# Kernel optimization log

Measured on AMD Instinct MI355X. Metric: run time of the kernel, lower is better.

The kernel has to match this reference:

```python
import jax, jax.numpy as jnp
import numpy as np

D_MODEL = 1024
N_HEAD = 16
DIM_PER_HEAD = D_MODEL // N_HEAD
B, S = 8, 1024


def setup_inputs() -> dict:
    key = jax.random.key(0)
    ks = jax.random.split(key, 12)
    s = 0.02
    return {
        "k": jax.random.normal(ks[0], (B, S, D_MODEL), jnp.float32),
        "v": jax.random.normal(ks[1], (B, S, D_MODEL), jnp.float32),
        "q": jax.random.normal(ks[2], (B, S, D_MODEL), jnp.float32),
        "attn_mask": jax.random.randint(ks[3], (B, S, S), 0, 2, jnp.int32),
        "Wk": jax.random.normal(ks[4], (D_MODEL, D_MODEL), jnp.float32) * s,
        "bk": jnp.zeros((D_MODEL,), jnp.float32),
        "Wv": jax.random.normal(ks[5], (D_MODEL, D_MODEL), jnp.float32) * s,
        "bv": jnp.zeros((D_MODEL,), jnp.float32),
        "Wq": jax.random.normal(ks[6], (D_MODEL, D_MODEL), jnp.float32) * s,
        "bq": jnp.zeros((D_MODEL,), jnp.float32),
        "Wo": jax.random.normal(ks[7], (D_MODEL, D_MODEL), jnp.float32) * s,
        "bo": jnp.zeros((D_MODEL,), jnp.float32),
    }


def reference(k, v, q, attn_mask, Wk, bk, Wv, bv, Wq, bq, Wo, bo):
    batch, key_len, _ = k.shape
    query_len = q.shape[1]
    scale = 1.0 / jnp.sqrt(jnp.float32(DIM_PER_HEAD))

    def split_heads(x):  # [b, s, d] -> [b, h, s, dh]
        return x.reshape(batch, -1, N_HEAD, DIM_PER_HEAD).transpose(0, 2, 1, 3)

    key_up = split_heads(k @ Wk + bk)
    value_up = split_heads(v @ Wv + bv)
    query_up = split_heads(q @ Wq + bq) * scale

    # [b, h, q, k] scores; mask nonzero entries with -inf (masked_fill_ semantics)
    scores = jnp.einsum("bhqd,bhkd->bhqk", query_up, key_up)
    scores = jnp.where(attn_mask[:, None, :, :] != 0, -jnp.inf, scores)
    attn = jax.nn.softmax(scores, axis=-1)
    # NOTE: original applies dropout but discards the result; attn (pre-dropout) is used.
    context = jnp.einsum("bhqk,bhkd->bhqd", attn, value_up)
    context = context.transpose(0, 2, 1, 3).reshape(batch, query_len, D_MODEL)
    output = context @ Wo + bo
    attn_mean = attn.sum(axis=1) / N_HEAD  # [b, q, k]
    return output, attn_mean
```

## Files before the change

kernel.cpp:

```cpp
#include <hip/hip_runtime.h>
#include <hip/hip_bf16.h>

typedef unsigned short u16;
typedef unsigned int u32;
typedef __attribute__((ext_vector_type(8))) short bf16x8;
typedef __attribute__((ext_vector_type(4))) float f32x4;
typedef __attribute__((ext_vector_type(4))) u16 u16x4;
typedef __attribute__((ext_vector_type(4))) u32 u32x4;

#define DEV static __device__ __forceinline__

DEV u16 f2bf(float x) {
  unsigned u = __builtin_bit_cast(unsigned, x);
  u += 0x7fffu + ((u >> 16) & 1u);
  return (u16)(u >> 16);
}
DEV float bf2f(u16 u) { return __builtin_bit_cast(float, ((unsigned)u) << 16); }

DEV u32 cvtpk(float lo, float hi) {
  u32 r;
  asm("v_cvt_pk_bf16_f32 %0, %1, %2" : "=v"(r) : "v"(lo), "v"(hi));
  return r;
}

DEV void glds16(const u16* g, u16* l) {
  __builtin_amdgcn_global_load_lds(
      (const __attribute__((address_space(1))) void*)g,
      (__attribute__((address_space(3))) void*)l, 16, 0, 0);
}

__global__ __launch_bounds__(256) void prep(
    const float* __restrict__ k, const float* __restrict__ v,
    const float* __restrict__ q,
    const float* __restrict__ w0, const float* __restrict__ w1,
    const float* __restrict__ w2, const float* __restrict__ w3,
    const int* __restrict__ mask,
    u16* __restrict__ Xb, u16* __restrict__ WT,
    unsigned long long* __restrict__ Mb) {
  __shared__ u16 tile[32][33];
  const int bid = (int)blockIdx.x;
  const int tid = threadIdx.x;
  if (bid < 2048) {
    const size_t i0 = (size_t)bid * 256 + tid;
    for (size_t t = i0; t < 6291456; t += 524288) {
      const size_t e = t * 4;
      const float* src = (e < 8388608) ? k + e
                       : (e < 16777216) ? v + (e - 8388608)
                       : q + (e - 16777216);
      const f32x4 x = *(const f32x4*)src;
      u16x4 o;
#pragma unroll
      for (int r = 0; r < 4; ++r) o[r] = f2bf(x[r]);
      *(u16x4*)&Xb[e] = o;
    }
  } else if (bid < 6144) {
    const int lb = bid - 2048;
    const int mat = lb >> 10;
    const int bx = lb & 1023;
    const float* in = (mat == 0) ? w0 : (mat == 1) ? w1 : (mat == 2) ? w2 : w3;
    u16* o = WT + (size_t)mat * 1048576;
    const int bk = (bx & 31) << 5;
    const int bn = (bx >> 5) << 5;
    const int tx = tid & 31, ty = tid >> 5;
#pragma unroll
    for (int i = 0; i < 32; i += 8)
      tile[ty + i][tx] = f2bf(in[(size_t)(bk + ty + i) * 1024 + bn + tx]);
    __syncthreads();
#pragma unroll
    for (int i = 0; i < 32; i += 8)
      o[(size_t)(bn + ty + i) * 1024 + bk + tx] = tile[tx][ty + i];
  } else {
    const int lb = bid - 6144;
    const int qt = lb & 63, b = lb >> 6;
    const int w = tid >> 6, l = tid & 63;
    const int ln = l & 15, lg = l >> 4;
    const int* Mp = mask + ((size_t)b << 20) + ((size_t)(qt << 4) << 10);
    unsigned long long m = 0ull;
#pragma unroll
    for (int t = 0; t < 16; ++t) {
      const int key = (w << 8) + (t << 4) + ln;
#pragma unroll
      for (int r = 0; r < 4; ++r) {
        const int row = (lg << 2) + r;
        if (Mp[((size_t)row << 10) + key] != 0) m |= 1ull << ((t << 2) + r);
      }
    }
    Mb[((((size_t)b << 6) + qt) << 8) + tid] = m;
  }
}

__global__ __launch_bounds__(256) void gemm_qkv(
    const u16* __restrict__ Xb, const u16* __restrict__ WTall,
    const float* __restrict__ bK, const float* __restrict__ bV,
    const float* __restrict__ bQ,
    u16* __restrict__ Kup, u16* __restrict__ VupT, u16* __restrict__ Qup) {
  __shared__ u16 As[8192];
  __shared__ u16 Bs[8192];
  const int mode = blockIdx.y;
  const u16* A = Xb + (size_t)mode * 8388608;
  const u16* Bw = WTall + (size_t)mode * 1048576;
  const float* bias = (mode == 0) ? bK : (mode == 1) ? bV : bQ;

  const int tid = threadIdx.x;
  const int w = tid >> 6, l = tid & 63;
  const int ln = l & 15, lg = l >> 4;
  const int wr = w >> 1, wc = w & 1;
  const int mb = ((int)blockIdx.x >> 3) << 7;
  const int nb = ((int)blockIdx.x & 7) << 7;

  f32x4 acc[4][4] = {};
  const int ar = (wr << 6) + ln;
  const int br = (wc << 6) + ln;
  const int x7 = ln & 7;

  for (int k0 = 0; k0 < 1024; k0 += 64) {
#pragma unroll
    for (int i = 0; i < 4; ++i) {
      const int off = (i << 11) + (tid << 3);
      const int row = off >> 6;
      const int sc = ((((off >> 3) & 7) ^ (row & 7)) << 3);
      glds16(A + (size_t)(mb + row) * 1024 + k0 + sc, As + off);
      glds16(Bw + (size_t)(nb + row) * 1024 + k0 + sc, Bs + off);
    }
    __syncthreads();
#pragma unroll
    for (int kk = 0; kk < 2; ++kk) {
      const int g = (kk << 2) + lg;
      const int rc = (g ^ x7) << 3;
      bf16x8 aa[4], bb[4];
#pragma unroll
      for (int mt = 0; mt < 4; ++mt) {
        aa[mt] = *(const bf16x8*)&As[(ar + (mt << 4)) * 64 + rc];
        bb[mt] = *(const bf16x8*)&Bs[(br + (mt << 4)) * 64 + rc];
      }
#pragma unroll
      for (int mt = 0; mt < 4; ++mt)
#pragma unroll
        for (int nt = 0; nt < 4; ++nt)
          acc[mt][nt] = __builtin_amdgcn_mfma_f32_16x16x32_bf16(aa[mt], bb[nt], acc[mt][nt], 0, 0, 0);
    }
    __syncthreads();
  }

  const float scale = (mode == 2) ? 0.125f : 1.0f;
#pragma unroll
  for (int mt = 0; mt < 4; ++mt) {
    const int m0 = mb + (wr << 6) + (mt << 4) + (lg << 2);
    const int bb_ = m0 >> 10, s0 = m0 & 1023;
#pragma unroll
    for (int nt = 0; nt < 4; ++nt) {
      const int n = nb + (wc << 6) + (nt << 4) + ln;
      const float bval = bias[n];
      const int h = n >> 6, dh = n & 63;
      const size_t bh = (size_t)(bb_ * 16 + h);
      if (mode == 1) {
        const int wv = dh >> 4, lnv = dh & 15;
        const int kk = s0 >> 5, lgv = (s0 >> 3) & 3, e0 = s0 & 7;
        u16x4 pk;
#pragma unroll
        for (int r = 0; r < 4; ++r) pk[r] = f2bf(acc[mt][nt][r] + bval);
        *(u16x4*)&VupT[(bh << 16) + (wv << 14) + (kk << 9) + (lgv << 7) +
                       (lnv << 3) + e0] = pk;
      } else if (mode == 0) {
        const int half = dh >> 5, lg2 = (dh >> 3) & 3, e = dh & 7;
        const int T = s0 >> 4;
        u16* base = Kup + (bh << 16) + (T << 10) + (half << 9) + (lg2 << 7) + e;
#pragma unroll
        for (int r = 0; r < 4; ++r)
          base[((s0 & 15) + r) << 3] = f2bf(acc[mt][nt][r] + bval);
      } else {
#pragma unroll
        for (int r = 0; r < 4; ++r)
          Qup[((bh << 10) + s0 + r) * 64 + dh] =
              f2bf((acc[mt][nt][r] + bval) * scale);
      }
    }
  }
}

__global__ __launch_bounds__(256) void gemm_out(
    const u16* __restrict__ Ctx, const u16* __restrict__ WTall,
    const float* __restrict__ bO, const u16* __restrict__ Pp,
    float* __restrict__ Out) {
  __shared__ u16 As[8192];
  __shared__ u16 Bs[8192];
  const int bid = (int)blockIdx.x;
  const int tid = threadIdx.x;

  if (bid >= 512) {
    float* Am = Out + 8388608;
    const size_t i = ((size_t)(bid - 512) * 256 + tid) * 8;
    const u16x4* q0 = (const u16x4*)&Pp[i];
    const u16x4* q1 = (const u16x4*)&Pp[8388608 + i];
    const u16x4 a0 = q0[0], a1 = q0[1], b0 = q1[0], b1 = q1[1];
    f32x4 lo, hi;
#pragma unroll
    for (int r = 0; r < 4; ++r) {
      lo[r] = (bf2f(a0[r]) + bf2f(b0[r])) * 0.0625f;
      hi[r] = (bf2f(a1[r]) + bf2f(b1[r])) * 0.0625f;
    }
    *(f32x4*)&Am[i] = lo;
    *(f32x4*)&Am[i + 4] = hi;
    return;
  }

  const u16* Bw = WTall + 3145728;
  const int w = tid >> 6, l = tid & 63;
  const int ln = l & 15, lg = l >> 4;
  const int wr = w >> 1, wc = w & 1;
  const int mb = (bid >> 3) << 7;
  const int nb = (bid & 7) << 7;

  f32x4 acc[4][4] = {};
  const int ar = (wr << 6) + ln;
  const int br = (wc << 6) + ln;
  const int x7 = ln & 7;

  for (int k0 = 0; k0 < 1024; k0 += 64) {
#pragma unroll
    for (int i = 0; i < 4; ++i) {
      const int off = (i << 11) + (tid << 3);
      const int row = off >> 6;
      const int sc = ((((off >> 3) & 7) ^ (row & 7)) << 3);
      glds16(Ctx + (size_t)(mb + row) * 1024 + k0 + sc, As + off);
      glds16(Bw + (size_t)(nb + row) * 1024 + k0 + sc, Bs + off);
    }
    __syncthreads();
#pragma unroll
    for (int kk = 0; kk < 2; ++kk) {
      const int g = (kk << 2) + lg;
      const int rc = (g ^ x7) << 3;
      bf16x8 aa[4], bb[4];
#pragma unroll
      for (int mt = 0; mt < 4; ++mt) {
        aa[mt] = *(const bf16x8*)&As[(ar + (mt << 4)) * 64 + rc];
        bb[mt] = *(const bf16x8*)&Bs[(br + (mt << 4)) * 64 + rc];
      }
#pragma unroll
      for (int mt = 0; mt < 4; ++mt)
#pragma unroll
        for (int nt = 0; nt < 4; ++nt)
          acc[mt][nt] = __builtin_amdgcn_mfma_f32_16x16x32_bf16(aa[mt], bb[nt], acc[mt][nt], 0, 0, 0);
    }
    __syncthreads();
  }
#pragma unroll
  for (int mt = 0; mt < 4; ++mt) {
    const int m0 = mb + (wr << 6) + (mt << 4) + (lg << 2);
#pragma unroll
    for (int nt = 0; nt < 4; ++nt) {
      const int n = nb + (wc << 6) + (nt << 4) + ln;
      const float bval = bO[n];
#pragma unroll
      for (int r = 0; r < 4; ++r)
        Out[(size_t)(m0 + r) * 1024 + n] = acc[mt][nt][r] + bval;
    }
  }
}

__global__ __launch_bounds__(256, 2) void attn_kernel(
    const u16* __restrict__ Qup, const u16* __restrict__ Kf,
    const u16* __restrict__ Vf, const unsigned long long* __restrict__ Mb,
    u16* __restrict__ Ctx, u16* __restrict__ Pp) {
  __shared__ u16 P_lds[16 * 1024];
  __shared__ float red_s[4][16];
  __shared__ float invs[16];

  const int tid = threadIdx.x;
  const int w = tid >> 6, l = tid & 63;
  const int ln = l & 15, lg = l >> 4;
  const int kg8 = lg << 3;

  const int bid = (int)blockIdx.x;
  const int b = bid & 7;
  const int idx = bid >> 3;
  const int qt = idx & 63;
  const int hs = idx >> 6;
  const int qb = qt << 4;

  const unsigned long long mbits = Mb[((((size_t)b << 6) + qt) << 8) + tid];

  u32x4 accp[8];

#pragma unroll 1
  for (int hh = 0; hh < 8; ++hh) {
    const int h = (hs << 3) + hh;
    const size_t bh = (size_t)(b * 16 + h);
    const u16* Qp = Qup + ((bh << 10) + qb) * 64;
    const u16* Kb = Kf + (bh << 16);
    const u16* Vb = Vf + (bh << 16) + ((size_t)w << 14);

    const bf16x8 qa0 = *(const bf16x8*)&Qp[ln * 64 + kg8];
    const bf16x8 qa1 = *(const bf16x8*)&Qp[ln * 64 + 32 + kg8];

    bf16x8 ka[3], kb[3];
#pragma unroll
    for (int p = 0; p < 3; ++p) {
      const int To = ((w << 4) + p) << 10;
      ka[p] = *(const bf16x8*)&Kb[To + (l << 3)];
      kb[p] = *(const bf16x8*)&Kb[To + 512 + (l << 3)];
    }

    float rsum[4] = {0, 0, 0, 0};
#pragma unroll
    for (int t = 0; t < 16; ++t) {
      const int s = t % 3;
      const bf16x8 k0 = ka[s], k1 = kb[s];
      if (t + 3 < 16) {
        const int To = ((w << 4) + t + 3) << 10;
        ka[s] = *(const bf16x8*)&Kb[To + (l << 3)];
        kb[s] = *(const bf16x8*)&Kb[To + 512 + (l << 3)];
      }
      f32x4 c = {0, 0, 0, 0};
      c = __builtin_amdgcn_mfma_f32_16x16x32_bf16(qa0, k0, c, 0, 0, 0);
      c = __builtin_amdgcn_mfma_f32_16x16x32_bf16(qa1, k1, c, 0, 0, 0);
      const int key = (w << 8) + (t << 4) + ln;
      float p[4];
#pragma unroll
      for (int r = 0; r < 4; ++r) {
        p[r] = ((mbits >> ((t << 2) + r)) & 1ull) ? 0.0f : __expf(c[r] - 4.0f);
        rsum[r] += p[r];
      }
      const u32 pk01 = cvtpk(p[0], p[1]);
      const u32 pk23 = cvtpk(p[2], p[3]);
      const int r0 = lg << 2;
      *(u16*)((char*)P_lds + ((((r0 + 0) << 11) + (key << 1)) ^ (((r0 + 0) & 7) << 4))) = (u16)pk01;
      *(u16*)((char*)P_lds + ((((r0 + 1) << 11) + (key << 1)) ^ (((r0 + 1) & 7) << 4))) = (u16)(pk01 >> 16);
      *(u16*)((char*)P_lds + ((((r0 + 2) << 11) + (key << 1)) ^ (((r0 + 2) & 7) << 4))) = (u16)pk23;
      *(u16*)((char*)P_lds + ((((r0 + 3) << 11) + (key << 1)) ^ (((r0 + 3) & 7) << 4))) = (u16)(pk23 >> 16);
    }
#pragma unroll
    for (int off = 1; off < 16; off <<= 1) {
#pragma unroll
      for (int r = 0; r < 4; ++r) rsum[r] += __shfl_xor(rsum[r], off);
    }
    if (ln == 0) {
#pragma unroll
      for (int r = 0; r < 4; ++r) red_s[w][(lg << 2) + r] = rsum[r];
    }

    bf16x8 vr[4];
#pragma unroll
    for (int p = 0; p < 4; ++p)
      vr[p] = *(const bf16x8*)&Vb[(p << 9) + (l << 3)];

    __syncthreads();
    float inv[4];
#pragma unroll
    for (int r = 0; r < 4; ++r) {
      const int row = (lg << 2) + r;
      inv[r] = 1.0f / (red_s[0][row] + red_s[1][row] + red_s[2][row] + red_s[3][row]);
    }
    if (ln == 0) {
#pragma unroll
      for (int r = 0; r < 4; ++r) invs[(lg << 2) + r] = inv[r];
    }

    f32x4 c0 = {0, 0, 0, 0}, c1 = {0, 0, 0, 0};
#pragma unroll
    for (int kk = 0; kk < 32; ++kk) {
      const int s = kk & 3;
      const bf16x8 vb = vr[s];
      if (kk + 4 < 32)
        vr[s] = *(const bf16x8*)&Vb[((kk + 4) << 9) + (l << 3)];
      const int a0 = ((ln << 11) + (((kk << 5) + kg8) << 1)) ^ ((ln & 7) << 4);
      const bf16x8 pa = *(const bf16x8*)((const char*)P_lds + a0);
      if (kk & 1)
        c1 = __builtin_amdgcn_mfma_f32_16x16x32_bf16(pa, vb, c1, 0, 0, 0);
      else
        c0 = __builtin_amdgcn_mfma_f32_16x16x32_bf16(pa, vb, c0, 0, 0, 0);
    }
    {
      const u32 q01 = cvtpk((c0[0] + c1[0]) * inv[0], (c0[1] + c1[1]) * inv[1]);
      const u32 q23 = cvtpk((c0[2] + c1[2]) * inv[2], (c0[3] + c1[3]) * inv[3]);
      u16* Cp = &Ctx[(((size_t)b << 10) + qb + (lg << 2)) * 1024 + (h << 6) + (w << 4) + ln];
      Cp[0] = (u16)q01;
      Cp[1024] = (u16)(q01 >> 16);
      Cp[2048] = (u16)q23;
      Cp[3072] = (u16)(q23 >> 16);
    }

    {
      const int row = tid >> 4;
      const float iv = invs[row];
#pragma unroll
      for (int i = 0; i < 8; ++i) {
        const int chunk = (tid & 15) + (i << 4);
        const int bo_ = ((row << 11) + (chunk << 4)) ^ ((row & 7) << 4);
        const u32x4 pu = *(const u32x4*)((const char*)P_lds + bo_);
        u32x4 o;
#pragma unroll
        for (int j = 0; j < 4; ++j) {
          const float plo = __builtin_bit_cast(float, pu[j] << 16) * iv;
          const float phi = __builtin_bit_cast(float, pu[j] & 0xFFFF0000u) * iv;
          if (hh == 0) {
            o[j] = cvtpk(plo, phi);
          } else {
            const u32 a = accp[i][j];
            const float alo = __builtin_bit_cast(float, a << 16);
            const float ahi = __builtin_bit_cast(float, a & 0xFFFF0000u);
            o[j] = cvtpk(alo + plo, ahi + phi);
          }
        }
        accp[i] = o;
      }
    }
    __syncthreads();
  }

  {
    const int row = tid >> 4;
    u16* Pg = Pp + ((size_t)hs << 23) + (((size_t)b << 10) + qb + row) * 1024;
#pragma unroll
    for (int i = 0; i < 8; ++i) {
      const int chunk = (tid & 15) + (i << 4);
      *(u32x4*)&Pg[chunk << 3] = accp[i];
    }
  }
}

extern "C" void kernel_launch(void* const* d_in, const int* in_sizes, int n_in,
                              void* d_out, int out_size, void* d_ws, size_t ws_size,
                              hipStream_t stream) {
  const float* k_in = (const float*)d_in[0];
  const float* v_in = (const float*)d_in[1];
  const float* q_in = (const float*)d_in[2];
  const int* mask = (const int*)d_in[3];
  const float* Wk = (const float*)d_in[4];
  const float* bk = (const float*)d_in[5];
  const float* Wv = (const float*)d_in[6];
  const float* bv = (const float*)d_in[7];
  const float* Wq = (const float*)d_in[8];
  const float* bq = (const float*)d_in[9];
  const float* Wo = (const float*)d_in[10];
  const float* bo = (const float*)d_in[11];

  float* out = (float*)d_out;

  u16* ws = (u16*)d_ws;
  u16* WT = ws;
  u16* Xb = ws + 4194304;
  unsigned long long* Mb = (unsigned long long*)(ws + 29360128);
  u16* Pp = ws + 37748736;
  u16* Kf   = ws + 71303168;
  u16* Vf   = ws + 79691776;
  u16* Qup  = ws + 88080384;
  u16* Ctx  = ws + 96468992;

  prep<<<6656, 256, 0, stream>>>(k_in, v_in, q_in, Wk, Wv, Wq, Wo, mask,
                                 Xb, WT, Mb);
  gemm_qkv<<<dim3(512, 3), dim3(256), 0, stream>>>(
      Xb, WT, bk, bv, bq, Kf, Vf, Qup);
  attn_kernel<<<dim3(1024), dim3(256), 0, stream>>>(
      Qup, Kf, Vf, Mb, Ctx, Pp);
  gemm_out<<<4608, 256, 0, stream>>>(Ctx, WT, bo, Pp, out);
}
```

Measured before the change: 297.9 us.

## Process 32 query rows per attention block to reuse K/V loads

Each attention block now handles two 16-row query tiles instead of one. The K and V fragments loaded from global memory feed MFMAs for both tiles, which halves K/V traffic per query row, and the grid is halved to 512 blocks. In exchange, LDS usage doubles to 64KB for P, the accp register array doubles, and fewer blocks may reduce occupancy and parallelism on the 256 CUs.

```diff
diff --git a/kernel.cpp b/kernel.cpp
--- a/kernel.cpp
+++ b/kernel.cpp
@@ -262,9 +262,9 @@
     const u16* __restrict__ Qup, const u16* __restrict__ Kf,
     const u16* __restrict__ Vf, const unsigned long long* __restrict__ Mb,
     u16* __restrict__ Ctx, u16* __restrict__ Pp) {
-  __shared__ u16 P_lds[16 * 1024];
-  __shared__ float red_s[4][16];
-  __shared__ float invs[16];
+  __shared__ u16 P_lds[32 * 1024];
+  __shared__ float red_s[4][32];
+  __shared__ float invs[32];
 
   const int tid = threadIdx.x;
   const int w = tid >> 6, l = tid & 63;
@@ -274,13 +274,14 @@
   const int bid = (int)blockIdx.x;
   const int b = bid & 7;
   const int idx = bid >> 3;
-  const int qt = idx & 63;
-  const int hs = idx >> 6;
-  const int qb = qt << 4;
-
-  const unsigned long long mbits = Mb[((((size_t)b << 6) + qt) << 8) + tid];
-
-  u32x4 accp[8];
+  const int qt = idx & 31;
+  const int hs = idx >> 5;
+  const int qb = qt << 5;
+
+  const unsigned long long mb_lo = Mb[((((size_t)b << 6) + (qt << 1)) << 8) + tid];
+  const unsigned long long mb_hi = Mb[((((size_t)b << 6) + (qt << 1) + 1) << 8) + tid];
+
+  u32x4 accp[16];
 
 #pragma unroll 1
   for (int hh = 0; hh < 8; ++hh) {
@@ -292,6 +293,8 @@
 
     const bf16x8 qa0 = *(const bf16x8*)&Qp[ln * 64 + kg8];
     const bf16x8 qa1 = *(const bf16x8*)&Qp[ln * 64 + 32 + kg8];
+    const bf16x8 qa2 = *(const bf16x8*)&Qp[(16 + ln) * 64 + kg8];
+    const bf16x8 qa3 = *(const bf16x8*)&Qp[(16 + ln) * 64 + 32 + kg8];
 
     bf16x8 ka[3], kb[3];
 #pragma unroll
@@ -301,7 +304,7 @@
       kb[p] = *(const bf16x8*)&Kb[To + 512 + (l << 3)];
     }
 
-    float rsum[4] = {0, 0, 0, 0};
+    float rsl[4] = {0, 0, 0, 0}, rsh[4] = {0, 0, 0, 0};
 #pragma unroll
     for (int t = 0; t < 16; ++t) {
       const int s = t % 3;
@@ -311,32 +314,54 @@
         ka[s] = *(const bf16x8*)&Kb[To + (l << 3)];
         kb[s] = *(const bf16x8*)&Kb[To + 512 + (l << 3)];
       }
-      f32x4 c = {0, 0, 0, 0};
-      c = __builtin_amdgcn_mfma_f32_16x16x32_bf16(qa0, k0, c, 0, 0, 0);
-      c = __builtin_amdgcn_mfma_f32_16x16x32_bf16(qa1, k1, c, 0, 0, 0);
+      f32x4 cl = {0, 0, 0, 0}, ch = {0, 0, 0, 0};
+      cl = __builtin_amdgcn_mfma_f32_16x16x32_bf16(qa0, k0, cl, 0, 0, 0);
+      ch = __builtin_amdgcn_mfma_f32_16x16x32_bf16(qa2, k0, ch, 0, 0, 0);
+      cl = __builtin_amdgcn_mfma_f32_16x16x32_bf16(qa1, k1, cl, 0, 0, 0);
+      ch = __builtin_amdgcn_mfma_f32_16x16x32_bf16(qa3, k1, ch, 0, 0, 0);
       const int key = (w << 8) + (t << 4) + ln;
-      float p[4];
+      float pl[4], ph[4];
 #pragma unroll
       for (int r = 0; r < 4; ++r) {
-        p[r] = ((mbits >> ((t << 2) + r)) & 1ull) ? 0.0f : __expf(c[r] - 4.0f);
-        rsum[r] += p[r];
-      }
-      const u32 pk01 = cvtpk(p[0], p[1]);
-      const u32 pk23 = cvtpk(p[2], p[3]);
+        pl[r] = ((mb_lo >> ((t << 2) + r)) & 1ull) ? 0.0f : __expf(cl[r] - 4.0f);
+        ph[r] = ((mb_hi >> ((t << 2) + r)) & 1ull) ? 0.0f : __expf(ch[r] - 4.0f);
+        rsl[r] += pl[r];
+        rsh[r] += ph[r];
+      }
+      const u32 l01 = cvtpk(pl[0], pl[1]);
+      const u32 l23 = cvtpk(pl[2], pl[3]);
+      const u32 h01 = cvtpk(ph[0], ph[1]);
+      const u32 h23 = cvtpk(ph[2], ph[3]);
       const int r0 = lg << 2;
-      *(u16*)((char*)P_lds + ((((r0 + 0) << 11) + (key << 1)) ^ (((r0 + 0) & 7) << 4))) = (u16)pk01;
-      *(u16*)((char*)P_lds + ((((r0 + 1) << 11) + (key << 1)) ^ (((r0 + 1) & 7) << 4))) = (u16)(pk01 >> 16);
-      *(u16*)((char*)P_lds + ((((r0 + 2) << 11) + (key << 1)) ^ (((r0 + 2) & 7) << 4))) = (u16)pk23;
-      *(u16*)((char*)P_lds + ((((r0 + 3) << 11) + (key << 1)) ^ (((r0 + 3) & 7) << 4))) = (u16)(pk23 >> 16);
+      const int x = (r0 & 7) << 4;
+#pragma unroll
+      for (int r = 0; r < 4; ++r) {
+        const int rowl = r0 + r;
+        const u16 vl = (u16)((r & 1) ? ((r < 2 ? l01 : l23) >> 16)
+                                     : (r < 2 ? l01 : l23));
+        *(u16*)((char*)P_lds +
+                (((rowl << 11) + (key << 1)) ^ ((rowl & 7) << 4))) = vl;
+        const int rowh = rowl + 16;
+        const u16 vh = (u16)((r & 1) ? ((r < 2 ? h01 : h23) >> 16)
+                                     : (r < 2 ? h01 : h23));
+        *(u16*)((char*)P_lds +
+                (((rowh << 11) + (key << 1)) ^ ((rowh & 7) << 4))) = vh;
+      }
     }
 #pragma unroll
     for (int off = 1; off < 16; off <<= 1) {
 #pragma unroll
-      for (int r = 0; r < 4; ++r) rsum[r] += __shfl_xor(rsum[r], off);
+      for (int r = 0; r < 4; ++r) {
+        rsl[r] += __shfl_xor(rsl[r], off);
+        rsh[r] += __shfl_xor(rsh[r], off);
+      }
     }
     if (ln == 0) {
 #pragma unroll
-      for (int r = 0; r < 4; ++r) red_s[w][(lg << 2) + r] = rsum[r];
+      for (int r = 0; r < 4; ++r) {
+        red_s[w][(lg << 2) + r] = rsl[r];
+        red_s[w][16 + (lg << 2) + r] = rsh[r];
+      }
     }
 
     bf16x8 vr[4];
@@ -345,64 +370,91 @@
       vr[p] = *(const bf16x8*)&Vb[(p << 9) + (l << 3)];
 
     __syncthreads();
-    float inv[4];
+    float invl[4], invh[4];
 #pragma unroll
     for (int r = 0; r < 4; ++r) {
       const int row = (lg << 2) + r;
-      inv[r] = 1.0f / (red_s[0][row] + red_s[1][row] + red_s[2][row] + red_s[3][row]);
+      invl[r] = 1.0f / (red_s[0][row] + red_s[1][row] + red_s[2][row] + red_s[3][row]);
+      invh[r] = 1.0f / (red_s[0][row + 16] + red_s[1][row + 16] +
+                        red_s[2][row + 16] + red_s[3][row + 16]);
     }
     if (ln == 0) {
 #pragma unroll
-      for (int r = 0; r < 4; ++r) invs[(lg << 2) + r] = inv[r];
+      for (int r = 0; r < 4; ++r) {
+        invs[(lg << 2) + r] = invl[r];
+        invs[16 + (lg << 2) + r] = invh[r];
+      }
     }
 
     f32x4 c0 = {0, 0, 0, 0}, c1 = {0, 0, 0, 0};
+    f32x4 c2 = {0, 0, 0, 0}, c3 = {0, 0, 0, 0};
 #pragma unroll
     for (int kk = 0; kk < 32; ++kk) {
       const int s = kk & 3;
       const bf16x8 vb = vr[s];
       if (kk + 4 < 32)
         vr[s] = *(const bf16x8*)&Vb[((kk + 4) << 9) + (l << 3)];
-      const int a0 = ((ln << 11) + (((kk << 5) + kg8) << 1)) ^ ((ln & 7) << 4);
-      const bf16x8 pa = *(const bf16x8*)((const char*)P_lds + a0);
-      if (kk & 1)
-        c1 = __builtin_amdgcn_mfma_f32_16x16x32_bf16(pa, vb, c1, 0, 0, 0);
-      else
-        c0 = __builtin_amdgcn_mfma_f32_16x16x32_bf16(pa, vb, c0, 0, 0, 0);
+      const int al = ((ln << 11) + (((kk << 5) + kg8) << 1)) ^ ((ln & 7) << 4);
+      const int ah = (((16 + ln) << 11) + (((kk << 5) + kg8) << 1)) ^ ((ln & 7) << 4);
+      const bf16x8 pal = *(const bf16x8*)((const char*)P_lds + al);
+      const bf16x8 pah = *(const bf16x8*)((const char*)P_lds + ah);
+      if (kk & 1) {
+        c1 = __builtin_amdgcn_mfma_f32_16x16x32_bf16(pal, vb, c1, 0, 0, 0);
+        c3 = __builtin_amdgcn_mfma_f32_16x16x32_bf16(pah, vb, c3, 0, 0, 0);
+      } else {
+        c0 = __builtin_amdgcn_mfma_f32_16x16x32_bf16(pal, vb, c0, 0, 0, 0);
+        c2 = __builtin_amdgcn_mfma_f32_16x16x32_bf16(pah, vb, c2, 0, 0, 0);
+      }
     }
     {
-      const u32 q01 = cvtpk((c0[0] + c1[0]) * inv[0], (c0[1] + c1[1]) * inv[1]);
-      const u32 q23 = cvtpk((c0[2] + c1[2]) * inv[2], (c0[3] + c1[3]) * inv[3]);
+      const u32 q01 = cvtpk((c0[0] + c1[0]) * invl[0], (c0[1] + c1[1]) * invl[1]);
+      const u32 q23 = cvtpk((c0[2] + c1[2]) * invl[2], (c0[3] + c1[3]) * invl[3]);
+      const u32 r01 = cvtpk((c2[0] + c3[0]) * invh[0], (c2[1] + c3[1]) * invh[1]);
+      const u32 r23 = cvtpk((c2[2] + c3[2]) * invh[2], (c2[3] + c3[3]) * invh[3]);
       u16* Cp = &Ctx[(((size_t)b << 10) + qb + (lg << 2)) * 1024 + (h << 6) + (w << 4) + ln];
       Cp[0] = (u16)q01;
       Cp[1024] = (u16)(q01 >> 16);
       Cp[2048] = (u16)q23;
       Cp[3072] = (u16)(q23 >> 16);
+      u16* Ch = Cp + 16 * 1024;
+      Ch[0] = (u16)r01;
+      Ch[1024] = (u16)(r01 >> 16);
+      Ch[2048] = (u16)r23;
+      Ch[3072] = (u16)(r23 >> 16);
     }
 
     {
       const int row = tid >> 4;
-      const float iv = invs[row];
+      const float ivl = invs[row];
+      const float ivh = invs[row + 16];
 #pragma unroll
       for (int i = 0; i < 8; ++i) {
         const int chunk = (tid & 15) + (i << 4);
-        const int bo_ = ((row << 11) + (chunk << 4)) ^ ((row & 7) << 4);
-        const u32x4 pu = *(const u32x4*)((const char*)P_lds + bo_);
-        u32x4 o;
+        const int bl = ((row << 11) + (chunk << 4)) ^ ((row & 7) << 4);
+        const int bhh = (((row + 16) << 11) + (chunk << 4)) ^ ((row & 7) << 4);
+        const u32x4 pu = *(const u32x4*)((const char*)P_lds + bl);
+        const u32x4 pv = *(const u32x4*)((const char*)P_lds + bhh);
+        u32x4 o, o2;
 #pragma unroll
         for (int j = 0; j < 4; ++j) {
-          const float plo = __builtin_bit_cast(float, pu[j] << 16) * iv;
-          const float phi = __builtin_bit_cast(float, pu[j] & 0xFFFF0000u) * iv;
+          const float plo = __builtin_bit_cast(float, pu[j] << 16) * ivl;
+          const float phi = __builtin_bit_cast(float, pu[j] & 0xFFFF0000u) * ivl;
+          const float qlo = __builtin_bit_cast(float, pv[j] << 16) * ivh;
+          const float qhi = __builtin_bit_cast(float, pv[j] & 0xFFFF0000u) * ivh;
           if (hh == 0) {
             o[j] = cvtpk(plo, phi);
+            o2[j] = cvtpk(qlo, qhi);
           } else {
             const u32 a = accp[i][j];
-            const float alo = __builtin_bit_cast(float, a << 16);
-            const float ahi = __builtin_bit_cast(float, a & 0xFFFF0000u);
-            o[j] = cvtpk(alo + plo, ahi + phi);
+            o[j] = cvtpk(__builtin_bit_cast(float, a << 16) + plo,
+                         __builtin_bit_cast(float, a & 0xFFFF0000u) + phi);
+            const u32 a2 = accp[i + 8][j];
+            o2[j] = cvtpk(__builtin_bit_cast(float, a2 << 16) + qlo,
+                          __builtin_bit_cast(float, a2 & 0xFFFF0000u) + qhi);
           }
         }
         accp[i] = o;
+        accp[i + 8] = o2;
       }
     }
     __syncthreads();
@@ -411,10 +463,12 @@
   {
     const int row = tid >> 4;
     u16* Pg = Pp + ((size_t)hs << 23) + (((size_t)b << 10) + qb + row) * 1024;
+    u16* Ph = Pg + 16 * 1024;
 #pragma unroll
     for (int i = 0; i < 8; ++i) {
       const int chunk = (tid & 15) + (i << 4);
       *(u32x4*)&Pg[chunk << 3] = accp[i];
+      *(u32x4*)&Ph[chunk << 3] = accp[i + 8];
     }
   }
 }
@@ -451,7 +505,7 @@
                                  Xb, WT, Mb);
   gemm_qkv<<<dim3(512, 3), dim3(256), 0, stream>>>(
       Xb, WT, bk, bv, bq, Kf, Vf, Qup);
-  attn_kernel<<<dim3(1024), dim3(256), 0, stream>>>(
+  attn_kernel<<<dim3(512), dim3(256), 0, stream>>>(
       Qup, Kf, Vf, Mb, Ctx, Pp);
   gemm_out<<<4608, 256, 0, stream>>>(Ctx, WT, bo, Pp, out);
 }
```

After: 462.4 us. 55.2% more time.
